# Optimization experiments

Measured on AMD Instinct MI355X. Metric: run time of the kernel, lower is better.

Reference implementation:

```python
import jax, jax.numpy as jnp
import numpy as np

B, S, D = 4, 2048, 1024

def setup_inputs() -> dict:
    key = jax.random.key(0)
    k0, k1, k2, k3, k4, k5 = jax.random.split(key, 6)
    scale = 1.0 / np.sqrt(D)
    return {
        "input_seq_embs": jax.random.normal(k0, (B, S, D), dtype=jnp.float32),
        "W_Q": jax.random.normal(k1, (D, D), dtype=jnp.float32) * scale,
        "W_K": jax.random.normal(k2, (D, D), dtype=jnp.float32) * scale,
        "W_V": jax.random.normal(k3, (D, D), dtype=jnp.float32) * scale,
        "W_O": jax.random.normal(k4, (D, D), dtype=jnp.float32) * scale,
        "b_O": jax.random.normal(k5, (D,), dtype=jnp.float32) * 0.01,
    }

def reference(input_seq_embs, W_Q, W_K, W_V, W_O, b_O):
    # torch nn.Linear: y = x @ W.T
    Q = jnp.einsum('bsd,ed->bse', input_seq_embs, W_Q)
    K = jnp.einsum('bsd,ed->bse', input_seq_embs, W_K)
    V = jnp.einsum('bsd,ed->bse', input_seq_embs, W_V)
    # NOTE: no 1/sqrt(d) scaling in the original module
    A = jnp.einsum('bqd,bkd->bqk', Q, K)  # [B,S,S]
    # log(tril(ones)) == 0 on/below diagonal, -inf above
    causal = jnp.tril(jnp.ones((S, S), dtype=bool))
    A = jnp.where(causal[None, :, :], A, -jnp.inf)
    A = jax.nn.softmax(A, axis=-1)
    # dropout layers are identity in eval mode
    out = jnp.einsum('bqk,bkd->bqd', A, V)
    out = jnp.einsum('bsd,ed->bse', out, W_O) + b_O
    return out
```

## Files before the change

### kernel.cpp

```cpp
#include <hip/hip_runtime.h>
#include <cstdint>

typedef _Float16 f16x8 __attribute__((ext_vector_type(8)));
typedef _Float16 f16x4 __attribute__((ext_vector_type(4)));
typedef float    f32x4 __attribute__((ext_vector_type(4)));

#define AS1 __attribute__((address_space(1)))
#define AS3 __attribute__((address_space(3)))

__device__ __forceinline__ void load16_lds(const void* g, void* l) {
  __builtin_amdgcn_global_load_lds((AS1 void*)g, (AS3 void*)l, 16, 0, 0);
}

#define GEMM_PROLOGUE(Ab, lda, Bb, ldb)                                   \
  __shared__ _Float16 lA[128 * 64];                                       \
  __shared__ _Float16 lB[128 * 64];                                       \
  int tid = threadIdx.x;                                                  \
  int srow = tid >> 3;                                                    \
  int gch = ((tid & 7) ^ (srow & 7)) * 8;                                 \
  const _Float16* gA = Ab + (long long)srow * (lda) + gch;                \
  const _Float16* gB = Bb + (long long)srow * (ldb) + gch;                \
  _Float16* lAw = lA + tid * 8;                                           \
  _Float16* lBw = lB + tid * 8;                                           \
  f32x4 acc[4][4] = {};                                                   \
  int lane = tid & 63;                                                    \
  int wv = tid >> 6;                                                      \
  int wm = (wv & 1) * 64, wn = (wv >> 1) * 64;                            \
  int l16 = lane & 15, quad = lane >> 4;                                  \
  int cswz = (quad ^ (l16 & 7)) * 8;                                      \
  int raw = (wm + l16) * 64 + cswz;                                       \
  int rbw = (wn + l16) * 64 + cswz;

#define GEMM_KLOOP(lda, ldb, KLEN, SWAP)                                  \
  for (int kb = 0; kb < (KLEN); kb += 64) {                               \
    __syncthreads();                                                      \
    load16_lds(gA,              lAw);                                     \
    load16_lds(gA + 32 * (lda), lAw + 2048);                              \
    load16_lds(gA + 64 * (lda), lAw + 4096);                              \
    load16_lds(gA + 96 * (lda), lAw + 6144);                              \
    load16_lds(gB,              lBw);                                     \
    load16_lds(gB + 32 * (ldb), lBw + 2048);                              \
    load16_lds(gB + 64 * (ldb), lBw + 4096);                              \
    load16_lds(gB + 96 * (ldb), lBw + 6144);                              \
    gA += 64; gB += 64;                                                   \
    __syncthreads();                                                      \
    _Pragma("unroll")                                                     \
    for (int s = 0; s < 2; s++) {                                         \
      int sx = s * 32;                                                    \
      f16x8 af[4], bfr[4];                                                \
      _Pragma("unroll")                                                   \
      for (int i = 0; i < 4; i++)                                         \
        af[i] = *(const f16x8*)(lA + ((raw + i * 1024) ^ sx));            \
      _Pragma("unroll")                                                   \
      for (int j = 0; j < 4; j++)                                         \
        bfr[j] = *(const f16x8*)(lB + ((rbw + j * 1024) ^ sx));           \
      _Pragma("unroll")                                                   \
      for (int i = 0; i < 4; i++)                                         \
        _Pragma("unroll")                                                 \
        for (int j = 0; j < 4; j++)                                       \
          acc[i][j] = (SWAP)                                              \
            ? __builtin_amdgcn_mfma_f32_16x16x32_f16(bfr[j], af[i], acc[i][j], 0, 0, 0) \
            : __builtin_amdgcn_mfma_f32_16x16x32_f16(af[i], bfr[j], acc[i][j], 0, 0, 0);\
    }                                                                     \
  }

__global__ __launch_bounds__(256) void cvt_all(
    const float* __restrict__ x, const float* __restrict__ wq,
    const float* __restrict__ wk, const float* __restrict__ wv,
    const float* __restrict__ wo,
    _Float16* __restrict__ xh, _Float16* __restrict__ wcat,
    _Float16* __restrict__ woh) {
  long long g = (long long)blockIdx.x * 256 + threadIdx.x;
  const float* in; _Float16* out; long long idx;
  if (g < 2097152)      { in = x;  out = xh;             idx = g; }
  else if (g < 2359296) { in = wq; out = wcat;           idx = g - 2097152; }
  else if (g < 2621440) { in = wk; out = wcat + 1048576; idx = g - 2359296; }
  else if (g < 2883584) { in = wv; out = wcat + 2097152; idx = g - 2621440; }
  else                  { in = wo; out = woh;            idx = g - 2883584; }
  float4 v = ((const float4*)in)[idx];
  f16x4 o;
  o[0] = (_Float16)v.x; o[1] = (_Float16)v.y; o[2] = (_Float16)v.z; o[3] = (_Float16)v.w;
  ((f16x4*)out)[idx] = o;
}

#define VMW(NLIT) asm volatile("s_waitcnt vmcnt(" #NLIT ")" ::: "memory")

#define A0R 0
#define B0R 16384
#define A1R 32768
#define B1R 49152

#define SGA(reg, u, kc) load16_lds(pA + (u) * 65536 + (kc), shm + (reg) + (u) * 4096 + tid * 8)
#define SGB(reg, u, kc) load16_lds(pB + (u) * 65536 + (kc), shm + (reg) + (u) * 4096 + tid * 8)

#define QPH(ABASE, BBASE, MQ, SWAP, STAGES, WAITS)                         \
  {                                                                        \
    if ((MQ) == 0) {                                                       \
      _Pragma("unroll")                                                    \
      for (int nf = 0; nf < 4; nf++) {                                     \
        int o = (BBASE) + rbw + nf * 1024;                                 \
        bf[nf][0] = *(const f16x8*)(shm + o);                              \
        bf[nf][1] = *(const f16x8*)(shm + (o ^ 32));                       \
      }                                                                    \
    }                                                                      \
    f16x8 af[2][2];                                                        \
    _Pragma("unroll")                                                      \
    for (int mi = 0; mi < 2; mi++) {                                       \
      int o = (ABASE) + raw + ((MQ) * 2 + mi) * 1024;                      \
      af[mi][0] = *(const f16x8*)(shm + o);                                \
      af[mi][1] = *(const f16x8*)(shm + (o ^ 32));                         \
    }                                                                      \
    STAGES                                                                 \
    WAITS                                                                  \
    __builtin_amdgcn_sched_barrier(0);                                     \
    __builtin_amdgcn_s_barrier();                                          \
    asm volatile("s_waitcnt lgkmcnt(0)" ::: "memory");                     \
    __builtin_amdgcn_sched_barrier(0);                                     \
    __builtin_amdgcn_s_setprio(1);                                         \
    _Pragma("unroll")                                                      \
    for (int ks = 0; ks < 2; ks++)                                         \
      _Pragma("unroll")                                                    \
      for (int mi = 0; mi < 2; mi++)                                       \
        _Pragma("unroll")                                                  \
        for (int nf = 0; nf < 4; nf++)                                     \
          acc[(MQ) * 2 + mi][nf] = (SWAP)                                  \
            ? __builtin_amdgcn_mfma_f32_16x16x32_f16(bf[nf][ks], af[mi][ks], acc[(MQ) * 2 + mi][nf], 0, 0, 0) \
            : __builtin_amdgcn_mfma_f32_16x16x32_f16(af[mi][ks], bf[nf][ks], acc[(MQ) * 2 + mi][nf], 0, 0, 0); \
    __builtin_amdgcn_s_setprio(0);                                         \
    __builtin_amdgcn_sched_barrier(0);                                     \
    __builtin_amdgcn_s_barrier();                                          \
  }

#define QKV_SETUP(APTR, BPTR)                                              \
  __shared__ _Float16 shm[65536];                                          \
  int tid = threadIdx.x;                                                   \
  const _Float16* pA = (APTR) + (long long)(tid >> 3) * 1024 +             \
                       ((tid & 7) ^ ((tid >> 3) & 7)) * 8;                 \
  const _Float16* pB = (BPTR) + (long long)(tid >> 3) * 1024 +             \
                       ((tid & 7) ^ ((tid >> 3) & 7)) * 8;                 \
  int lane = tid & 63, wv = tid >> 6;                                      \
  int wr = wv & 1, wc = wv >> 1;                                           \
  int l16 = lane & 15, quad = lane >> 4;                                   \
  int cswz = (quad ^ (l16 & 7)) * 8;                                       \
  int raw = (wr * 128 + l16) * 64 + cswz;                                  \
  int rbw = (wc * 64 + l16) * 64 + cswz;                                   \
  f32x4 acc[8][4] = {};

#define QKV_PRO()                                                          \
  SGB(B0R, 0, 0); SGB(B0R, 1, 0); SGB(B0R, 2, 0); SGB(B0R, 3, 0);          \
  SGA(A0R, 0, 0); SGA(A0R, 1, 0); SGA(A0R, 2, 0); SGA(A0R, 3, 0);          \
  SGB(B1R, 0, 64); SGB(B1R, 1, 64); SGB(B1R, 2, 64); SGB(B1R, 3, 64);      \
  SGA(A1R, 0, 64); SGA(A1R, 2, 64);                                        \
  VMW(6);                                                                  \
  __builtin_amdgcn_s_barrier();

#define QKV_MAIN(SWAP)                                                     \
  _Pragma("unroll 1")                                                      \
  for (int it = 0; it < 7; ++it) {                                         \
    int kb = it * 128;                                                     \
    f16x8 bf[4][2];                                                        \
    QPH(A0R, B0R, 0, SWAP, { SGA(A1R, 1, kb + 64);  SGA(A1R, 3, kb + 64); }, {})  \
    QPH(A0R, B0R, 1, SWAP, { SGB(B0R, 0, kb + 128); SGB(B0R, 1, kb + 128); }, {}) \
    QPH(A0R, B0R, 2, SWAP, { SGB(B0R, 2, kb + 128); SGB(B0R, 3, kb + 128); }, {}) \
    QPH(A0R, B0R, 3, SWAP, { SGA(A0R, 0, kb + 128); SGA(A0R, 2, kb + 128); }, { VMW(6); }) \
    QPH(A1R, B1R, 0, SWAP, { SGA(A0R, 1, kb + 128); SGA(A0R, 3, kb + 128); }, {}) \
    QPH(A1R, B1R, 1, SWAP, { SGB(B1R, 0, kb + 192); SGB(B1R, 1, kb + 192); }, {}) \
    QPH(A1R, B1R, 2, SWAP, { SGB(B1R, 2, kb + 192); SGB(B1R, 3, kb + 192); }, {}) \
    QPH(A1R, B1R, 3, SWAP, { SGA(A1R, 0, kb + 192); SGA(A1R, 2, kb + 192); }, { VMW(6); }) \
  }                                                                        \
  {                                                                        \
    f16x8 bf[4][2];                                                        \
    QPH(A0R, B0R, 0, SWAP, { SGA(A1R, 1, 960); SGA(A1R, 3, 960); }, {})    \
    QPH(A0R, B0R, 1, SWAP, {}, {})                                         \
    QPH(A0R, B0R, 2, SWAP, {}, {})                                         \
    QPH(A0R, B0R, 3, SWAP, {}, { VMW(0); })                                \
    QPH(A1R, B1R, 0, SWAP, {}, {})                                         \
    QPH(A1R, B1R, 1, SWAP, {}, {})                                         \
    QPH(A1R, B1R, 2, SWAP, {}, {})                                         \
    QPH(A1R, B1R, 3, SWAP, {}, {})                                         \
  }

__global__ __launch_bounds__(512, 2) void qkv_qk(
    const _Float16* __restrict__ A, const _Float16* __restrict__ B,
    _Float16* __restrict__ Qh, _Float16* __restrict__ Kh) {
  int bid = blockIdx.x;
  int swz = (bid & 7) * 32 + (bid >> 3);
  int by = swz >> 3, bx = swz & 7;
  QKV_SETUP(A + (long long)by * 262144, B + (long long)bx * 262144)
  QKV_PRO()
  QKV_MAIN(1)
  _Float16* C = (bx < 4) ? Qh : Kh;
  int m0 = by * 256 + wr * 128 + l16;
  int n0 = (bx & 3) * 256 + wc * 64 + quad * 4;
  #pragma unroll
  for (int i = 0; i < 8; i++)
    #pragma unroll
    for (int j = 0; j < 4; j++) {
      f16x4 pk;
      #pragma unroll
      for (int r = 0; r < 4; r++) pk[r] = (_Float16)acc[i][j][r];
      *(f16x4*)(C + (long long)(m0 + i * 16) * 1024 + (n0 + j * 16)) = pk;
    }
}

__global__ __launch_bounds__(512, 2) void qkv_v(
    const _Float16* __restrict__ A, const _Float16* __restrict__ B,
    _Float16* __restrict__ Vt) {
  int bid = blockIdx.x;
  int swz = (bid & 7) * 16 + (bid >> 3);
  int by = swz >> 2, bx = swz & 3;
  QKV_SETUP(A + (long long)by * 262144, B + (long long)(bx + 8) * 262144)
  QKV_PRO()
  QKV_MAIN(0)
  int d0 = bx * 256 + wc * 64 + l16;
  int mg0 = by * 256 + wr * 128 + quad * 4;
  #pragma unroll
  for (int i = 0; i < 8; i++) {
    long long mg = mg0 + i * 16;
    long long b = mg >> 11;
    long long s = mg & 2047;
    #pragma unroll
    for (int j = 0; j < 4; j++) {
      f16x4 pk;
      #pragma unroll
      for (int r = 0; r < 4; r++) pk[r] = (_Float16)acc[i][j][r];
      *(f16x4*)(Vt + (b << 21) + (long long)(d0 + j * 16) * 2048 + s) = pk;
    }
  }
}

__global__ __launch_bounds__(256) void scores_gemm(
    const _Float16* __restrict__ Qh, const _Float16* __restrict__ Kh,
    _Float16* __restrict__ S, float2* __restrict__ stats) {
  int L = blockIdx.x;
  int xcd = L & 7;
  int bz = xcd >> 1;
  int t = (L >> 3) + (xcd & 1) * 136;
  int g = (int)((__builtin_sqrtf(4.0f * t + 1.0f) - 1.0f) * 0.5f);
  while ((g + 1) * (g + 2) <= t) g++;
  while (g * (g + 1) > t) g--;
  int rem = t - g * (g + 1);
  int by = 2 * g + (rem > g ? 1 : 0);
  int bxt = (rem > g) ? rem - (g + 1) : rem;
  bool diag = (bxt == g);

  const _Float16* Ab = Qh + (long long)bz * 2097152 + (long long)by * 64 * 1024;
  const _Float16* Bb = Kh + (long long)bz * 2097152 + (long long)bxt * 128 * 1024;

  __shared__ _Float16 lA[64 * 64];
  __shared__ _Float16 lB[128 * 64];
  __shared__ float redM[4][64];
  __shared__ float redL[4][64];

  int tid = threadIdx.x;
  int srow = tid >> 3;
  int gch = ((tid & 7) ^ (srow & 7)) * 8;
  const _Float16* gA = Ab + (long long)srow * 1024 + gch;
  const _Float16* gB = Bb + (long long)srow * 1024 + gch;
  _Float16* lAw = lA + tid * 8;
  _Float16* lBw = lB + tid * 8;

  f32x4 acc[4][2] = {};
  int lane = tid & 63;
  int wv = tid >> 6;
  int wn = wv * 32;
  int l16 = lane & 15, quad = lane >> 4;
  int cswz = (quad ^ (l16 & 7)) * 8;
  int raw = l16 * 64 + cswz;
  int rbw = (wn + l16) * 64 + cswz;

  for (int kb = 0; kb < 1024; kb += 64) {
    __syncthreads();
    load16_lds(gA,             lAw);
    load16_lds(gA + 32 * 1024, lAw + 2048);
    load16_lds(gB,             lBw);
    load16_lds(gB + 32 * 1024, lBw + 2048);
    load16_lds(gB + 64 * 1024, lBw + 4096);
    load16_lds(gB + 96 * 1024, lBw + 6144);
    gA += 64; gB += 64;
    __syncthreads();
    #pragma unroll
    for (int s = 0; s < 2; s++) {
      int sx = s * 32;
      f16x8 af[4], bfr[2];
      #pragma unroll
      for (int i = 0; i < 4; i++)
        af[i] = *(const f16x8*)(lA + ((raw + i * 1024) ^ sx));
      #pragma unroll
      for (int j = 0; j < 2; j++)
        bfr[j] = *(const f16x8*)(lB + ((rbw + j * 1024) ^ sx));
      #pragma unroll
      for (int i = 0; i < 4; i++)
        #pragma unroll
        for (int j = 0; j < 2; j++)
          acc[i][j] = __builtin_amdgcn_mfma_f32_16x16x32_f16(bfr[j], af[i], acc[i][j], 0, 0, 0);
    }
  }

  int rowBase = by * 64;
  int colBase = bxt * 128;

  float mloc[4];
  #pragma unroll
  for (int i = 0; i < 4; i++) {
    int grow = rowBase + 16 * i + l16;
    float mx = -3.0e38f;
    #pragma unroll
    for (int j = 0; j < 2; j++)
      #pragma unroll
      for (int r = 0; r < 4; r++) {
        bool ok = !diag || (colBase + wn + 16 * j + quad * 4 + r <= grow);
        mx = ok ? fmaxf(mx, acc[i][j][r]) : mx;
      }
    mx = fmaxf(mx, __shfl_xor(mx, 16));
    mx = fmaxf(mx, __shfl_xor(mx, 32));
    mloc[i] = mx;
  }
  if (quad == 0) {
    #pragma unroll
    for (int i = 0; i < 4; i++) redM[wv][16 * i + l16] = mloc[i];
  }
  __syncthreads();
  float mfin[4];
  #pragma unroll
  for (int i = 0; i < 4; i++) {
    int rl = 16 * i + l16;
    mfin[i] = fmaxf(fmaxf(redM[0][rl], redM[1][rl]), fmaxf(redM[2][rl], redM[3][rl]));
  }

  float lloc[4];
  #pragma unroll
  for (int i = 0; i < 4; i++) {
    int grow = rowBase + 16 * i + l16;
    float sum = 0.f;
    #pragma unroll
    for (int j = 0; j < 2; j++)
      #pragma unroll
      for (int r = 0; r < 4; r++) {
        bool ok = !diag || (colBase + wn + 16 * j + quad * 4 + r <= grow);
        float e = __expf(acc[i][j][r] - mfin[i]);
        sum += ok ? e : 0.f;
      }
    sum += __shfl_xor(sum, 16);
    sum += __shfl_xor(sum, 32);
    lloc[i] = sum;
  }
  if (quad == 0) {
    #pragma unroll
    for (int i = 0; i < 4; i++) redL[wv][16 * i + l16] = lloc[i];
  }
  __syncthreads();
  if (wv == 0 && quad == 0) {
    #pragma unroll
    for (int i = 0; i < 4; i++) {
      int rl = 16 * i + l16;
      float lt = redL[0][rl] + redL[1][rl] + redL[2][rl] + redL[3][rl];
      stats[((long long)bz * 2048 + rowBase + rl) * 16 + bxt] =
          make_float2(mfin[i], lt);
    }
  }

  _Float16* Sb = S + (long long)bz * 4194304;
  #pragma unroll
  for (int i = 0; i < 4; i++) {
    long long grow = rowBase + 16 * i + l16;
    #pragma unroll
    for (int j = 0; j < 2; j++) {
      f16x4 u;
      #pragma unroll
      for (int r = 0; r < 4; r++) u[r] = (_Float16)(acc[i][j][r] - mfin[i]);
      *(f16x4*)(Sb + grow * 2048 + (colBase + wn + 16 * j + quad * 4)) = u;
    }
  }
}

__global__ __launch_bounds__(256) void normalize_p(_Float16* __restrict__ S,
                                                   const float2* __restrict__ stats) {
  int g = blockIdx.x;
  int bz = g >> 11, row = g & 2047;
  int nt = (row >> 7) + 1;
  _Float16* srow = S + ((long long)bz * 2048 + row) * 2048;
  const float2* st = stats + ((long long)bz * 2048 + row) * 16;
  __shared__ float sh_invl;
  __shared__ float shd[16];
  int t = threadIdx.x;
  if (t < 16) {
    float2 p = (t < nt) ? st[t] : make_float2(-3.0e38f, 0.f);
    float m = p.x;
    #pragma unroll
    for (int d = 1; d < 16; d <<= 1) m = fmaxf(m, __shfl_xor(m, d));
    float term = p.y * __expf(p.x - m);
    #pragma unroll
    for (int d = 1; d < 16; d <<= 1) term += __shfl_xor(term, d);
    shd[t] = p.x - m;
    if (t == 0) sh_invl = 1.0f / term;
  }
  __syncthreads();
  float invl = sh_invl;
  int Lp = nt << 7;
  for (int c = t; (c << 3) < Lp; c += 256) {
    float dt = shd[c >> 4];
    f16x8 v = ((f16x8*)srow)[c];
    f16x8 o;
    int col0 = c << 3;
    #pragma unroll
    for (int e = 0; e < 8; e++) {
      float u = (float)v[e];
      float pe = __expf(u + dt) * invl;
      o[e] = (col0 + e <= row) ? (_Float16)pe : (_Float16)0.f;
    }
    ((f16x8*)srow)[c] = o;
  }
}

__global__ __launch_bounds__(256) void pv_splitk(
    const _Float16* __restrict__ P,
    const _Float16* __restrict__ Vt,
    float* __restrict__ P0, float* __restrict__ P1,
    _Float16* __restrict__ Oh) {
  int bid = blockIdx.x;
  int xcd = bid & 7;
  int bz = xcd >> 1;
  int idx = bid >> 3;
  int cy = idx >> 2;
  int bx = (xcd & 1) * 4 + (idx & 3);
  int by, c;
  if (cy < 8) { by = cy; c = 0; }
  else { int q = cy - 8; by = 8 + (q >> 1); c = q & 1; }
  int kmax = (by + 1) * 128;
  int k0 = c * 1024;
  int klen = min(kmax, k0 + 1024) - k0;

  const _Float16* Ab = P + (long long)bz * 4194304LL + (long long)by * 128 * 2048 + k0;
  const _Float16* Bb = Vt + (long long)bz * 2097152LL + (long long)bx * 128 * 2048 + k0;
  GEMM_PROLOGUE(Ab, 2048, Bb, 2048)
  GEMM_KLOOP(2048, 2048, klen, true)

  int m0 = by * 128 + wm + l16;
  int n0 = bx * 128 + wn + quad * 4;

  if (c == 0 && by < 8) {
    _Float16* C = Oh + (long long)bz * 2097152LL;
    #pragma unroll
    for (int i = 0; i < 4; i++)
      #pragma unroll
      for (int j = 0; j < 4; j++) {
        f16x4 pk;
        #pragma unroll
        for (int r = 0; r < 4; r++) pk[r] = (_Float16)acc[i][j][r];
        *(f16x4*)(C + (long long)(m0 + i * 16) * 1024 + (n0 + j * 16)) = pk;
      }
  } else if (c == 0) {
    float* C = P0 + (long long)bz * 2097152LL;
    #pragma unroll
    for (int i = 0; i < 4; i++)
      #pragma unroll
      for (int j = 0; j < 4; j++)
        *(f32x4*)(C + (long long)(m0 + i * 16) * 1024 + (n0 + j * 16)) = acc[i][j];
  } else {
    float* C = P1 + (long long)bz * 1048576LL;
    int mr = m0 - 1024;
    #pragma unroll
    for (int i = 0; i < 4; i++)
      #pragma unroll
      for (int j = 0; j < 4; j++)
        *(f32x4*)(C + (long long)(mr + i * 16) * 1024 + (n0 + j * 16)) = acc[i][j];
  }
}

__global__ __launch_bounds__(256) void pv_reduce(const float* __restrict__ P0,
                                                 const float* __restrict__ P1,
                                                 _Float16* __restrict__ Oh) {
  int i = blockIdx.x * 256 + threadIdx.x;
  if (i >= 1048576) return;
  int f4 = i;
  int bz = f4 >> 18;
  int loc = f4 & 262143;
  long long p0i = (long long)bz * 524288 + 262144 + loc;
  float4 v = ((const float4*)P0)[p0i];
  float4 w = ((const float4*)P1)[f4];
  v.x += w.x; v.y += w.y; v.z += w.z; v.w += w.w;
  f16x4 o;
  o[0] = (_Float16)v.x; o[1] = (_Float16)v.y; o[2] = (_Float16)v.z; o[3] = (_Float16)v.w;
  ((f16x4*)Oh)[p0i] = o;
}

__global__ __launch_bounds__(256) void oproj_gemm(
    const _Float16* __restrict__ A, const _Float16* __restrict__ B,
    float* __restrict__ C, const float* __restrict__ bias) {
  int bx = blockIdx.x, by = blockIdx.y;
  const _Float16* Ab = A + (long long)by * 128 * 1024;
  const _Float16* Bb = B + (long long)bx * 128 * 1024;
  GEMM_PROLOGUE(Ab, 1024, Bb, 1024)
  GEMM_KLOOP(1024, 1024, 1024, true)

  int m0 = by * 128 + wm + l16;
  int n0 = bx * 128 + wn + quad * 4;
  #pragma unroll
  for (int j = 0; j < 4; j++) {
    float4 b4 = *(const float4*)(bias + n0 + j * 16);
    #pragma unroll
    for (int i = 0; i < 4; i++) {
      f32x4 v = acc[i][j];
      v[0] += b4.x; v[1] += b4.y; v[2] += b4.z; v[3] += b4.w;
      *(f32x4*)(C + (long long)(m0 + i * 16) * 1024 + (n0 + j * 16)) = v;
    }
  }
}


extern "C" void kernel_launch(void* const* d_in, const int* in_sizes, int n_in,
                              void* d_out, int out_size, void* d_ws, size_t ws_size,
                              hipStream_t stream) {
  const float* x  = (const float*)d_in[0];
  const float* Wq = (const float*)d_in[1];
  const float* Wk = (const float*)d_in[2];
  const float* Wv = (const float*)d_in[3];
  const float* Wo = (const float*)d_in[4];
  const float* bO = (const float*)d_in[5];

  char* ws = (char*)d_ws;
  _Float16* xh   = (_Float16*)(ws + 0);
  _Float16* Wcat = (_Float16*)(ws + 16777216);
  _Float16* Woh  = (_Float16*)(ws + 23068672);
  _Float16* Qh   = (_Float16*)(ws + 25165824);
  _Float16* Kh   = (_Float16*)(ws + 41943040);
  _Float16* Vt   = (_Float16*)(ws + 58720256);
  _Float16* Oh   = (_Float16*)(ws + 75497472);
  _Float16* Sb   = (_Float16*)(ws + 92274688);
  float2*   stats= (float2*)  (ws + 125829120);
  float*    P0   = (float*)   (ws + 25165824);
  float*    P1   = (float*)   (ws + 0);

  dim3 blk(256);

  cvt_all<<<12288, blk, 0, stream>>>(x, Wq, Wk, Wv, Wo, xh, Wcat, Woh);

  qkv_qk<<<256, dim3(512), 0, stream>>>(xh, Wcat, Qh, Kh);
  qkv_v<<<128, dim3(512), 0, stream>>>(xh, Wcat, Vt);

  scores_gemm<<<1088, blk, 0, stream>>>(Qh, Kh, Sb, stats);

  normalize_p<<<8192, blk, 0, stream>>>(Sb, stats);

  pv_splitk<<<768, blk, 0, stream>>>(Sb, Vt, P0, P1, Oh);
  pv_reduce<<<4096, blk, 0, stream>>>(P0, P1, Oh);

  oproj_gemm<<<dim3(8, 64, 1), blk, 0, stream>>>(Oh, Woh, (float*)d_out, bO);
}
```

Baseline: 275.9 us.

## Fuse softmax exponent into scores GEMM and apply per-tile scaling in PV

The scores kernel now writes exp(s - tile_max) with the causal mask applied, and the separate normalize pass over the full P matrix is replaced by a tiny kernel that builds a per-row, per-tile scale table. The PV GEMM loads this table into LDS and multiplies each A fragment by its tile's scale before the MFMA. This removes a full read-modify-write pass over the half-precision score matrix. The scores kernel's LDS layout also changes from XOR-swizzled to split k-halves without swizzle, which may add LDS bank conflicts. The extra per-fragment multiply in the PV inner loop adds ALU work.

Result: no change. 279.6 us (+1.4%).

```diff
diff --git a/kernel.cpp b/kernel.cpp
--- a/kernel.cpp
+++ b/kernel.cpp
@@ -247,48 +247,49 @@
   const _Float16* Ab = Qh + (long long)bz * 2097152 + (long long)by * 64 * 1024;
   const _Float16* Bb = Kh + (long long)bz * 2097152 + (long long)bxt * 128 * 1024;
 
-  __shared__ _Float16 lA[64 * 64];
-  __shared__ _Float16 lB[128 * 64];
+  __shared__ _Float16 lA[2 * 64 * 32];
+  __shared__ _Float16 lB[2 * 128 * 32];
   __shared__ float redM[4][64];
   __shared__ float redL[4][64];
 
   int tid = threadIdx.x;
-  int srow = tid >> 3;
-  int gch = ((tid & 7) ^ (srow & 7)) * 8;
-  const _Float16* gA = Ab + (long long)srow * 1024 + gch;
-  const _Float16* gB = Bb + (long long)srow * 1024 + gch;
-  _Float16* lAw = lA + tid * 8;
-  _Float16* lBw = lB + tid * 8;
+  int r0 = tid >> 2;
+  int c0 = (tid & 3) * 8;
+  const _Float16* ga0 = Ab + (long long)r0 * 1024 + c0;
+  const _Float16* gb0 = Bb + (long long)r0 * 1024 + c0;
+  const _Float16* gb1 = Bb + (long long)(r0 + 64) * 1024 + c0;
+  _Float16* la0 = lA + tid * 8;
+  _Float16* la1 = lA + 2048 + tid * 8;
+  _Float16* lb0 = lB + tid * 8;
+  _Float16* lb1 = lB + 2048 + tid * 8;
+  _Float16* lb2 = lB + 4096 + tid * 8;
+  _Float16* lb3 = lB + 6144 + tid * 8;
 
   f32x4 acc[4][2] = {};
   int lane = tid & 63;
   int wv = tid >> 6;
   int wn = wv * 32;
   int l16 = lane & 15, quad = lane >> 4;
-  int cswz = (quad ^ (l16 & 7)) * 8;
-  int raw = l16 * 64 + cswz;
-  int rbw = (wn + l16) * 64 + cswz;
+  const _Float16* raBase = lA + l16 * 32 + quad * 8;
+  const _Float16* rbBase = lB + (wn + l16) * 32 + quad * 8;
 
   for (int kb = 0; kb < 1024; kb += 64) {
     __syncthreads();
-    load16_lds(gA,             lAw);
-    load16_lds(gA + 32 * 1024, lAw + 2048);
-    load16_lds(gB,             lBw);
-    load16_lds(gB + 32 * 1024, lBw + 2048);
-    load16_lds(gB + 64 * 1024, lBw + 4096);
-    load16_lds(gB + 96 * 1024, lBw + 6144);
-    gA += 64; gB += 64;
+    load16_lds(ga0, la0);
+    load16_lds(ga0 + 32, la1);
+    load16_lds(gb0, lb0);
+    load16_lds(gb1, lb1);
+    load16_lds(gb0 + 32, lb2);
+    load16_lds(gb1 + 32, lb3);
+    ga0 += 64; gb0 += 64; gb1 += 64;
     __syncthreads();
     #pragma unroll
     for (int s = 0; s < 2; s++) {
-      int sx = s * 32;
       f16x8 af[4], bfr[2];
       #pragma unroll
-      for (int i = 0; i < 4; i++)
-        af[i] = *(const f16x8*)(lA + ((raw + i * 1024) ^ sx));
-      #pragma unroll
-      for (int j = 0; j < 2; j++)
-        bfr[j] = *(const f16x8*)(lB + ((rbw + j * 1024) ^ sx));
+      for (int i = 0; i < 4; i++) af[i] = *(const f16x8*)(raBase + s * 2048 + i * 512);
+      #pragma unroll
+      for (int j = 0; j < 2; j++) bfr[j] = *(const f16x8*)(rbBase + s * 4096 + j * 512);
       #pragma unroll
       for (int i = 0; i < 4; i++)
         #pragma unroll
@@ -368,54 +369,50 @@
     for (int j = 0; j < 2; j++) {
       f16x4 u;
       #pragma unroll
-      for (int r = 0; r < 4; r++) u[r] = (_Float16)(acc[i][j][r] - mfin[i]);
+      for (int r = 0; r < 4; r++) {
+        bool ok = !diag || (colBase + wn + 16 * j + quad * 4 + r <= grow);
+        float pe = ok ? __expf(acc[i][j][r] - mfin[i]) : 0.f;
+        u[r] = (_Float16)pe;
+      }
       *(f16x4*)(Sb + grow * 2048 + (colBase + wn + 16 * j + quad * 4)) = u;
     }
   }
 }
 
-__global__ __launch_bounds__(256) void normalize_p(_Float16* __restrict__ S,
-                                                   const float2* __restrict__ stats) {
-  int g = blockIdx.x;
-  int bz = g >> 11, row = g & 2047;
-  int nt = (row >> 7) + 1;
-  _Float16* srow = S + ((long long)bz * 2048 + row) * 2048;
-  const float2* st = stats + ((long long)bz * 2048 + row) * 16;
-  __shared__ float sh_invl;
-  __shared__ float shd[16];
-  int t = threadIdx.x;
-  if (t < 16) {
-    float2 p = (t < nt) ? st[t] : make_float2(-3.0e38f, 0.f);
-    float m = p.x;
-    #pragma unroll
-    for (int d = 1; d < 16; d <<= 1) m = fmaxf(m, __shfl_xor(m, d));
-    float term = p.y * __expf(p.x - m);
-    #pragma unroll
-    for (int d = 1; d < 16; d <<= 1) term += __shfl_xor(term, d);
-    shd[t] = p.x - m;
-    if (t == 0) sh_invl = 1.0f / term;
-  }
-  __syncthreads();
-  float invl = sh_invl;
-  int Lp = nt << 7;
-  for (int c = t; (c << 3) < Lp; c += 256) {
-    float dt = shd[c >> 4];
-    f16x8 v = ((f16x8*)srow)[c];
-    f16x8 o;
-    int col0 = c << 3;
-    #pragma unroll
-    for (int e = 0; e < 8; e++) {
-      float u = (float)v[e];
-      float pe = __expf(u + dt) * invl;
-      o[e] = (col0 + e <= row) ? (_Float16)pe : (_Float16)0.f;
-    }
-    ((f16x8*)srow)[c] = o;
-  }
+__global__ __launch_bounds__(256) void alpha_tab(const float2* __restrict__ stats,
+                                                 _Float16* __restrict__ alpha) {
+  int row = blockIdx.x * 256 + threadIdx.x;
+  if (row >= 8192) return;
+  int r = row & 2047;
+  int nt = (r >> 7) + 1;
+  const float2* st = stats + (long long)row * 16;
+  float2 sv[16];
+  float M = -3.0e38f;
+  #pragma unroll
+  for (int t = 0; t < 16; t++) {
+    sv[t] = (t < nt) ? st[t] : make_float2(-3.0e38f, 0.f);
+    M = fmaxf(M, sv[t].x);
+  }
+  float Lsum = 0.f;
+  #pragma unroll
+  for (int t = 0; t < 16; t++) Lsum += sv[t].y * __expf(sv[t].x - M);
+  float invL = 1.0f / Lsum;
+  f16x8 o0, o1;
+  #pragma unroll
+  for (int t = 0; t < 8; t++)
+    o0[t] = (_Float16)((t < nt) ? __expf(sv[t].x - M) * invL : 0.f);
+  #pragma unroll
+  for (int t = 8; t < 16; t++)
+    o1[t - 8] = (_Float16)((t < nt) ? __expf(sv[t].x - M) * invL : 0.f);
+  f16x8* dst = (f16x8*)(alpha + (long long)row * 16);
+  dst[0] = o0;
+  dst[1] = o1;
 }
 
 __global__ __launch_bounds__(256) void pv_splitk(
     const _Float16* __restrict__ P,
     const _Float16* __restrict__ Vt,
+    const _Float16* __restrict__ alpha,
     float* __restrict__ P0, float* __restrict__ P1,
     _Float16* __restrict__ Oh) {
   int bid = blockIdx.x;
@@ -433,8 +430,64 @@
 
   const _Float16* Ab = P + (long long)bz * 4194304LL + (long long)by * 128 * 2048 + k0;
   const _Float16* Bb = Vt + (long long)bz * 2097152LL + (long long)bx * 128 * 2048 + k0;
-  GEMM_PROLOGUE(Ab, 2048, Bb, 2048)
-  GEMM_KLOOP(2048, 2048, klen, true)
+
+  __shared__ _Float16 lA[128 * 64];
+  __shared__ _Float16 lB[128 * 64];
+  __shared__ _Float16 lAl[2048];
+  int tid = threadIdx.x;
+  int srow = tid >> 3;
+  int gch = ((tid & 7) ^ (srow & 7)) * 8;
+  const _Float16* gA = Ab + (long long)srow * 2048 + gch;
+  const _Float16* gB = Bb + (long long)srow * 2048 + gch;
+  _Float16* lAw = lA + tid * 8;
+  _Float16* lBw = lB + tid * 8;
+  f32x4 acc[4][4] = {};
+  int lane = tid & 63;
+  int wv = tid >> 6;
+  int wm = (wv & 1) * 64, wn = (wv >> 1) * 64;
+  int l16 = lane & 15, quad = lane >> 4;
+  int cswz = (quad ^ (l16 & 7)) * 8;
+  int raw = (wm + l16) * 64 + cswz;
+  int rbw = (wn + l16) * 64 + cswz;
+
+  load16_lds(alpha + ((long long)bz * 2048 + by * 128) * 16 + tid * 8, lAl + tid * 8);
+
+  for (int kb = 0; kb < klen; kb += 64) {
+    __syncthreads();
+    load16_lds(gA,             lAw);
+    load16_lds(gA + 32 * 2048, lAw + 2048);
+    load16_lds(gA + 64 * 2048, lAw + 4096);
+    load16_lds(gA + 96 * 2048, lAw + 6144);
+    load16_lds(gB,             lBw);
+    load16_lds(gB + 32 * 2048, lBw + 2048);
+    load16_lds(gB + 64 * 2048, lBw + 4096);
+    load16_lds(gB + 96 * 2048, lBw + 6144);
+    gA += 64; gB += 64;
+    __syncthreads();
+    int kt = (k0 + kb) >> 7;
+    _Float16 av[4];
+    #pragma unroll
+    for (int i = 0; i < 4; i++)
+      av[i] = lAl[(wm + 16 * i + l16) * 16 + kt];
+    #pragma unroll
+    for (int s = 0; s < 2; s++) {
+      int sx = s * 32;
+      f16x8 af[4], bfr[4];
+      #pragma unroll
+      for (int i = 0; i < 4; i++) {
+        af[i] = *(const f16x8*)(lA + ((raw + i * 1024) ^ sx));
+        af[i] = af[i] * av[i];
+      }
+      #pragma unroll
+      for (int j = 0; j < 4; j++)
+        bfr[j] = *(const f16x8*)(lB + ((rbw + j * 1024) ^ sx));
+      #pragma unroll
+      for (int i = 0; i < 4; i++)
+        #pragma unroll
+        for (int j = 0; j < 4; j++)
+          acc[i][j] = __builtin_amdgcn_mfma_f32_16x16x32_f16(bfr[j], af[i], acc[i][j], 0, 0, 0);
+    }
+  }
 
   int m0 = by * 128 + wm + l16;
   int n0 = bx * 128 + wn + quad * 4;
@@ -529,6 +582,7 @@
   _Float16* Oh   = (_Float16*)(ws + 75497472);
   _Float16* Sb   = (_Float16*)(ws + 92274688);
   float2*   stats= (float2*)  (ws + 125829120);
+  _Float16* alpha= (_Float16*)(ws + 16777216);
   float*    P0   = (float*)   (ws + 25165824);
   float*    P1   = (float*)   (ws + 0);
 
@@ -541,9 +595,9 @@
 
   scores_gemm<<<1088, blk, 0, stream>>>(Qh, Kh, Sb, stats);
 
-  normalize_p<<<8192, blk, 0, stream>>>(Sb, stats);
-
-  pv_splitk<<<768, blk, 0, stream>>>(Sb, Vt, P0, P1, Oh);
+  alpha_tab<<<32, blk, 0, stream>>>(stats, alpha);
+
+  pv_splitk<<<768, blk, 0, stream>>>(Sb, Vt, alpha, P0, P1, Oh);
   pv_reduce<<<4096, blk, 0, stream>>>(P0, P1, Oh);
 
   oproj_gemm<<<dim3(8, 64, 1), blk, 0, stream>>>(Oh, Woh, (float*)d_out, bO);
```

## Move exp and causal mask into scores epilogue; restructure LDS layout as k-halves

Applied to the files above, without the earlier changes.

The scores GEMM now applies exp(s - m_tile) and the causal mask in its epilogue, storing unnormalized probabilities. The normalize pass then only multiplies each element by a per-tile factor exp(m_tile - m)/l, removing exps and compares from a memory-bound pass. Separately, the LDS tiles are laid out as two 32-wide k-halves without an XOR swizzle, which simplifies addressing but may bring back LDS bank conflicts. Storing exp values in fp16 instead of shifted logits also changes where precision is lost.

Result: no change. 281.0 us (+1.8%).

```diff
diff --git a/kernel.cpp b/kernel.cpp
--- a/kernel.cpp
+++ b/kernel.cpp
@@ -247,48 +247,49 @@
   const _Float16* Ab = Qh + (long long)bz * 2097152 + (long long)by * 64 * 1024;
   const _Float16* Bb = Kh + (long long)bz * 2097152 + (long long)bxt * 128 * 1024;
 
-  __shared__ _Float16 lA[64 * 64];
-  __shared__ _Float16 lB[128 * 64];
+  __shared__ _Float16 lA[2 * 64 * 32];
+  __shared__ _Float16 lB[2 * 128 * 32];
   __shared__ float redM[4][64];
   __shared__ float redL[4][64];
 
   int tid = threadIdx.x;
-  int srow = tid >> 3;
-  int gch = ((tid & 7) ^ (srow & 7)) * 8;
-  const _Float16* gA = Ab + (long long)srow * 1024 + gch;
-  const _Float16* gB = Bb + (long long)srow * 1024 + gch;
-  _Float16* lAw = lA + tid * 8;
-  _Float16* lBw = lB + tid * 8;
+  int r0 = tid >> 2;
+  int c0 = (tid & 3) * 8;
+  const _Float16* ga0 = Ab + (long long)r0 * 1024 + c0;
+  const _Float16* gb0 = Bb + (long long)r0 * 1024 + c0;
+  const _Float16* gb1 = Bb + (long long)(r0 + 64) * 1024 + c0;
+  _Float16* la0 = lA + tid * 8;
+  _Float16* la1 = lA + 2048 + tid * 8;
+  _Float16* lb0 = lB + tid * 8;
+  _Float16* lb1 = lB + 2048 + tid * 8;
+  _Float16* lb2 = lB + 4096 + tid * 8;
+  _Float16* lb3 = lB + 6144 + tid * 8;
 
   f32x4 acc[4][2] = {};
   int lane = tid & 63;
   int wv = tid >> 6;
   int wn = wv * 32;
   int l16 = lane & 15, quad = lane >> 4;
-  int cswz = (quad ^ (l16 & 7)) * 8;
-  int raw = l16 * 64 + cswz;
-  int rbw = (wn + l16) * 64 + cswz;
+  const _Float16* raBase = lA + l16 * 32 + quad * 8;
+  const _Float16* rbBase = lB + (wn + l16) * 32 + quad * 8;
 
   for (int kb = 0; kb < 1024; kb += 64) {
     __syncthreads();
-    load16_lds(gA,             lAw);
-    load16_lds(gA + 32 * 1024, lAw + 2048);
-    load16_lds(gB,             lBw);
-    load16_lds(gB + 32 * 1024, lBw + 2048);
-    load16_lds(gB + 64 * 1024, lBw + 4096);
-    load16_lds(gB + 96 * 1024, lBw + 6144);
-    gA += 64; gB += 64;
+    load16_lds(ga0, la0);
+    load16_lds(ga0 + 32, la1);
+    load16_lds(gb0, lb0);
+    load16_lds(gb1, lb1);
+    load16_lds(gb0 + 32, lb2);
+    load16_lds(gb1 + 32, lb3);
+    ga0 += 64; gb0 += 64; gb1 += 64;
     __syncthreads();
     #pragma unroll
     for (int s = 0; s < 2; s++) {
-      int sx = s * 32;
       f16x8 af[4], bfr[2];
       #pragma unroll
-      for (int i = 0; i < 4; i++)
-        af[i] = *(const f16x8*)(lA + ((raw + i * 1024) ^ sx));
-      #pragma unroll
-      for (int j = 0; j < 2; j++)
-        bfr[j] = *(const f16x8*)(lB + ((rbw + j * 1024) ^ sx));
+      for (int i = 0; i < 4; i++) af[i] = *(const f16x8*)(raBase + s * 2048 + i * 512);
+      #pragma unroll
+      for (int j = 0; j < 2; j++) bfr[j] = *(const f16x8*)(rbBase + s * 4096 + j * 512);
       #pragma unroll
       for (int i = 0; i < 4; i++)
         #pragma unroll
@@ -368,7 +369,11 @@
     for (int j = 0; j < 2; j++) {
       f16x4 u;
       #pragma unroll
-      for (int r = 0; r < 4; r++) u[r] = (_Float16)(acc[i][j][r] - mfin[i]);
+      for (int r = 0; r < 4; r++) {
+        bool ok = !diag || (colBase + wn + 16 * j + quad * 4 + r <= grow);
+        float pe = ok ? __expf(acc[i][j][r] - mfin[i]) : 0.f;
+        u[r] = (_Float16)pe;
+      }
       *(f16x4*)(Sb + grow * 2048 + (colBase + wn + 16 * j + quad * 4)) = u;
     }
   }
@@ -381,8 +386,7 @@
   int nt = (row >> 7) + 1;
   _Float16* srow = S + ((long long)bz * 2048 + row) * 2048;
   const float2* st = stats + ((long long)bz * 2048 + row) * 16;
-  __shared__ float sh_invl;
-  __shared__ float shd[16];
+  __shared__ float sha[16];
   int t = threadIdx.x;
   if (t < 16) {
     float2 p = (t < nt) ? st[t] : make_float2(-3.0e38f, 0.f);
@@ -392,23 +396,16 @@
     float term = p.y * __expf(p.x - m);
     #pragma unroll
     for (int d = 1; d < 16; d <<= 1) term += __shfl_xor(term, d);
-    shd[t] = p.x - m;
-    if (t == 0) sh_invl = 1.0f / term;
+    sha[t] = __expf(p.x - m) * (1.0f / term);
   }
   __syncthreads();
-  float invl = sh_invl;
   int Lp = nt << 7;
   for (int c = t; (c << 3) < Lp; c += 256) {
-    float dt = shd[c >> 4];
+    float sc = sha[c >> 4];
     f16x8 v = ((f16x8*)srow)[c];
     f16x8 o;
-    int col0 = c << 3;
-    #pragma unroll
-    for (int e = 0; e < 8; e++) {
-      float u = (float)v[e];
-      float pe = __expf(u + dt) * invl;
-      o[e] = (col0 + e <= row) ? (_Float16)pe : (_Float16)0.f;
-    }
+    #pragma unroll
+    for (int e = 0; e < 8; e++) o[e] = (_Float16)((float)v[e] * sc);
     ((f16x8*)srow)[c] = o;
   }
 }
```
